# Performance work log

Hardware: AMD Instinct MI355X
Metric: run time of the kernel (lower is better)

## Reference

```python
import jax, jax.numpy as jnp
import numpy as np

B, S, D = 2, 2048, 1024
H, DH = 16, 64
INNER = H * DH  # 1024
FF = 4 * D
WINDOW = 128
EPS = 1e-5
SCALE = DH ** -0.5


def setup_inputs() -> dict:
    key = jax.random.key(0)
    ks = jax.random.split(key, 8)
    s = lambda fan_in: 1.0 / np.sqrt(fan_in)
    return {
        "x": jax.random.normal(ks[0], (B, S, D), dtype=jnp.float32),
        "ln1_g": jnp.ones((D,), jnp.float32),
        "ln1_b": jnp.zeros((D,), jnp.float32),
        "w_qkv": jax.random.uniform(ks[1], (3 * INNER, D), jnp.float32, -s(D), s(D)),
        "w_out": jax.random.uniform(ks[2], (D, INNER), jnp.float32, -s(INNER), s(INNER)),
        "b_out": jnp.zeros((D,), jnp.float32),
        "ln2_g": jnp.ones((D,), jnp.float32),
        "ln2_b": jnp.zeros((D,), jnp.float32),
        "w_ff1": jax.random.uniform(ks[3], (FF, D), jnp.float32, -s(D), s(D)),
        "b_ff1": jnp.zeros((FF,), jnp.float32),
        "w_ff2": jax.random.uniform(ks[4], (D, FF), jnp.float32, -s(FF), s(FF)),
        "b_ff2": jnp.zeros((D,), jnp.float32),
    }


def _layernorm(x, g, b):
    mu = jnp.mean(x, axis=-1, keepdims=True)
    var = jnp.mean(jnp.square(x - mu), axis=-1, keepdims=True)
    return (x - mu) * jax.lax.rsqrt(var + EPS) * g + b


def reference(x, ln1_g, ln1_b, w_qkv, w_out, b_out, ln2_g, ln2_b, w_ff1, b_ff1, w_ff2, b_ff2):
    # --- attention block ---
    residual = x
    h = _layernorm(x, ln1_g, ln1_b)
    qkv = h @ w_qkv.T                             # [B, S, 3*INNER]
    q, k, v = jnp.split(qkv, 3, axis=-1)
    reshape_heads = lambda t: t.reshape(B, S, H, DH).transpose(0, 2, 1, 3)  # [B,H,S,DH]
    q, k, v = map(reshape_heads, (q, k, v))
    q = q * SCALE
    scores = jnp.einsum("bhqd,bhkd->bhqk", q, k)  # dense [B,H,S,S]
    # local sparse pattern: attend iff |i-j| <= window_size
    idx = jnp.arange(S)
    local_mask = jnp.abs(idx[:, None] - idx[None, :]) <= WINDOW  # [S,S] bool
    scores = jnp.where(local_mask[None, None], scores, -jnp.inf)
    attn = jax.nn.softmax(scores, axis=-1)
    attn = jnp.nan_to_num(attn, nan=0.0)
    out = jnp.einsum("bhqk,bhkd->bhqd", attn, v)  # [B,H,S,DH]
    out = out.transpose(0, 2, 1, 3).reshape(B, S, INNER)
    out = out @ w_out.T + b_out                   # dropout inactive (eval)
    x = residual + out
    # --- FFN block ---
    residual = x
    h = _layernorm(x, ln2_g, ln2_b)
    h = jax.nn.gelu(h @ w_ff1.T + b_ff1, approximate=False)
    h = h @ w_ff2.T + b_ff2
    return residual + h
```

## Files before the change

### kernel.cpp

```cpp
#include <hip/hip_runtime.h>
#include <stdint.h>

#define SEQ    2048
#define NB     2
#define DMODEL 1024
#define NHEAD  16
#define HDIM   64
#define FFDIM  4096
#define WIN    128
#define MTOK   (NB*SEQ)

typedef short short8 __attribute__((ext_vector_type(8)));
typedef float f32x4  __attribute__((ext_vector_type(4)));

__device__ __forceinline__ float bf2f(uint16_t h){ return __uint_as_float(((uint32_t)h) << 16); }
__device__ __forceinline__ uint16_t f2bf(float f){
  uint32_t u = __float_as_uint(f);
  u += 0x7fffu + ((u >> 16) & 1u);
  return (uint16_t)(u >> 16);
}

__device__ __forceinline__ float gelu_f(float v){
  float u = 0.7978845608028654f * v * (1.0f + 0.044715f * v * v);
  u = fminf(fmaxf(u, -10.0f), 10.0f);
  const float e = __expf(2.0f * u);
  const float th = (e - 1.0f) / (e + 1.0f);
  return 0.5f * v * (1.0f + th);
}

__device__ __forceinline__ void gl_lds16(const void* g, void* l) {
  __builtin_amdgcn_global_load_lds((const __attribute__((address_space(1))) void*)g,
                                   (__attribute__((address_space(3))) void*)l, 16, 0, 0);
}

__global__ __launch_bounds__(256) void cvtln_kernel(
    const float* __restrict__ s0, const float* __restrict__ s1,
    const float* __restrict__ s2, const float* __restrict__ s3,
    uint16_t* __restrict__ d0, uint16_t* __restrict__ d1,
    uint16_t* __restrict__ d2, uint16_t* __restrict__ d3,
    const float* __restrict__ x, const float* __restrict__ g,
    const float* __restrict__ b, uint16_t* __restrict__ y)
{
  __shared__ float red[8];
  const int t = threadIdx.x;
  if (blockIdx.x < 12288) {
    size_t i = (size_t)blockIdx.x * 256 + t;
    const float* s; uint16_t* d; size_t off;
    if      (i <  768*1024) { s = s0; d = d0; off = i; }
    else if (i < 1024*1024) { s = s1; d = d1; off = i -  768*1024; }
    else if (i < 2048*1024) { s = s2; d = d2; off = i - 1024*1024; }
    else                    { s = s3; d = d3; off = i - 2048*1024; }
    const float4 v = ((const float4*)s)[off];
    uint2 o;
    o.x = (uint32_t)f2bf(v.x) | ((uint32_t)f2bf(v.y) << 16);
    o.y = (uint32_t)f2bf(v.z) | ((uint32_t)f2bf(v.w) << 16);
    ((uint2*)d)[off] = o;
  } else {
    const int row = blockIdx.x - 12288;
    const float4 v = ((const float4*)(x + (size_t)row * DMODEL))[t];
    float s1 = v.x + v.y + v.z + v.w;
    float s2 = v.x*v.x + v.y*v.y + v.z*v.z + v.w*v.w;
    #pragma unroll
    for (int off = 32; off; off >>= 1) { s1 += __shfl_xor(s1, off, 64); s2 += __shfl_xor(s2, off, 64); }
    const int w = t >> 6;
    if ((t & 63) == 0) { red[w] = s1; red[4+w] = s2; }
    __syncthreads();
    s1 = red[0]+red[1]+red[2]+red[3];
    s2 = red[4]+red[5]+red[6]+red[7];
    const float mu = s1 * (1.0f/DMODEL);
    const float var = s2 * (1.0f/DMODEL) - mu*mu;
    const float rs = rsqrtf(var + 1e-5f);
    const float4 gv = ((const float4*)g)[t];
    const float4 bv = ((const float4*)b)[t];
    uint2 o;
    o.x = (uint32_t)f2bf((v.x-mu)*rs*gv.x + bv.x) | ((uint32_t)f2bf((v.y-mu)*rs*gv.y + bv.y) << 16);
    o.y = (uint32_t)f2bf((v.z-mu)*rs*gv.z + bv.z) | ((uint32_t)f2bf((v.w-mu)*rs*gv.w + bv.w) << 16);
    ((uint2*)(y + (size_t)row * DMODEL))[t] = o;
  }
}

__global__ __launch_bounds__(256) void ln_kernel(const float* __restrict__ x,
                                                 const float* __restrict__ g,
                                                 const float* __restrict__ b,
                                                 uint16_t* __restrict__ y)
{
  const int row = blockIdx.x;
  const int t = threadIdx.x;
  const float4 v = ((const float4*)(x + (size_t)row * DMODEL))[t];
  float s1 = v.x + v.y + v.z + v.w;
  float s2 = v.x*v.x + v.y*v.y + v.z*v.z + v.w*v.w;
  #pragma unroll
  for (int off = 32; off; off >>= 1) { s1 += __shfl_xor(s1, off, 64); s2 += __shfl_xor(s2, off, 64); }
  __shared__ float red[8];
  const int w = t >> 6;
  if ((t & 63) == 0) { red[w] = s1; red[4+w] = s2; }
  __syncthreads();
  s1 = red[0]+red[1]+red[2]+red[3];
  s2 = red[4]+red[5]+red[6]+red[7];
  const float mu = s1 * (1.0f/DMODEL);
  const float var = s2 * (1.0f/DMODEL) - mu*mu;
  const float rs = rsqrtf(var + 1e-5f);
  const float4 gv = ((const float4*)g)[t];
  const float4 bv = ((const float4*)b)[t];
  uint2 o;
  o.x = (uint32_t)f2bf((v.x-mu)*rs*gv.x + bv.x) | ((uint32_t)f2bf((v.y-mu)*rs*gv.y + bv.y) << 16);
  o.y = (uint32_t)f2bf((v.z-mu)*rs*gv.z + bv.z) | ((uint32_t)f2bf((v.w-mu)*rs*gv.w + bv.w) << 16);
  ((uint2*)(y + (size_t)row * DMODEL))[t] = o;
}

template<int EPI>
__global__ __launch_bounds__(512, 2) void gemm256(
    const uint16_t* __restrict__ A, const uint16_t* __restrict__ Bm,
    const float* __restrict__ bias, uint16_t* __restrict__ C,
    uint16_t* __restrict__ vt, int M, int N, int K)
{
  __shared__ __align__(16) uint16_t L[4 * 16384];
  const int t = threadIdx.x;
  const int l = t & 63;
  const int w = t >> 6;
  const int wm = w >> 2, wn = w & 3;
  const int GX = gridDim.x;
  const int nblk = GX * gridDim.y;
  const int lin  = blockIdx.y * GX + blockIdx.x;
  const int nid  = (lin & 7) * (nblk >> 3) + (lin >> 3);
  const int row0 = (nid / GX) * 256, col0 = (nid % GX) * 256;
  const int mrow = l & 15, kq = l >> 4;
  const int nt = K >> 5;

  f32x4 acc[8][4];
  #pragma unroll
  for (int i = 0; i < 8; ++i)
    #pragma unroll
    for (int j = 0; j < 4; ++j)
      #pragma unroll
      for (int e = 0; e < 4; ++e) acc[i][j][e] = 0.0f;

  const int sr = t >> 2;
  const int kl = (t & 3) ^ ((t >> 3) & 3);
  const uint16_t* aG = A  + (size_t)(row0 + sr) * K + kl * 8;
  const uint16_t* bG = Bm + (size_t)(col0 + sr) * K + kl * 8;
  char* const lds = (char*)L;
  const int soff = t * 16;

  #define STAGE_A(tt_) { char* d_ = lds + ((tt_) & 3) * 32768 + soff; \
      gl_lds16(aG + (tt_) * 32, d_); \
      gl_lds16(aG + (size_t)128 * K + (tt_) * 32, d_ + 8192); }
  #define STAGE_B(tt_) { char* d_ = lds + ((tt_) & 3) * 32768 + 16384 + soff; \
      gl_lds16(bG + (tt_) * 32, d_); \
      gl_lds16(bG + (size_t)128 * K + (tt_) * 32, d_ + 8192); }

  STAGE_A(0); STAGE_B(0);
  STAGE_A(1); STAGE_B(1);
  STAGE_A(2); STAGE_B(2);
  asm volatile("s_waitcnt vmcnt(8)");
  __builtin_amdgcn_s_barrier();

  const int cphys = (kq ^ ((mrow >> 1) & 3)) << 4;

  for (int tt = 0; tt < nt; ++tt) {
    char* const bufA = lds + (tt & 3) * 32768;
    char* const bufB = bufA + 16384;
    short8 bf[4], af[8];
    #pragma unroll
    for (int ni = 0; ni < 4; ++ni)
      bf[ni] = *(const short8*)(bufB + (wn*64 + ni*16 + mrow) * 64 + cphys);
    #pragma unroll
    for (int mi = 0; mi < 8; ++mi)
      af[mi] = *(const short8*)(bufA + (wm*128 + mi*16 + mrow) * 64 + cphys);
    if (tt + 3 < nt) {
      STAGE_A(tt + 3);
      STAGE_B(tt + 3);
      asm volatile("s_waitcnt vmcnt(8)");
    } else if (tt + 3 == nt) {
      asm volatile("s_waitcnt vmcnt(4)");
    } else if (tt + 2 == nt) {
      asm volatile("s_waitcnt vmcnt(0)");
    }
    __builtin_amdgcn_s_barrier();
    __builtin_amdgcn_s_setprio(1);
    #pragma unroll
    for (int mi = 0; mi < 8; ++mi)
      #pragma unroll
      for (int ni = 0; ni < 4; ++ni)
        acc[mi][ni] = __builtin_amdgcn_mfma_f32_16x16x32_bf16(af[mi], bf[ni], acc[mi][ni], 0, 0, 0);
    __builtin_amdgcn_s_setprio(0);
    __builtin_amdgcn_s_barrier();
  }
  #undef STAGE_A
  #undef STAGE_B

  const int crow = kq * 4;
  if (EPI == 1 && col0 >= 2048) {
    const int hd0 = col0 - 2048 + wn*64 + mrow;
    #pragma unroll
    for (int mi = 0; mi < 8; ++mi) {
      #pragma unroll
      for (int r = 0; r < 4; ++r) {
        const int row = row0 + wm*128 + mi*16 + crow + r;
        const int bb = row >> 11, ss = row & 2047;
        uint16_t* vr = vt + ((size_t)bb << 21) + ss;
        #pragma unroll
        for (int ni = 0; ni < 4; ++ni)
          vr[(size_t)(hd0 + ni*16) << 11] = f2bf(acc[mi][ni][r]);
      }
    }
  } else {
    float bv[4];
    #pragma unroll
    for (int ni = 0; ni < 4; ++ni)
      bv[ni] = (EPI == 2) ? bias[col0 + wn*64 + ni*16 + mrow] : 0.0f;
    #pragma unroll
    for (int mi = 0; mi < 8; ++mi) {
      #pragma unroll
      for (int r = 0; r < 4; ++r) {
        const int row = row0 + wm*128 + mi*16 + crow + r;
        uint16_t* Cr = C + (size_t)row * N + col0 + wn*64 + mrow;
        #pragma unroll
        for (int ni = 0; ni < 4; ++ni) {
          float v = acc[mi][ni][r] + bv[ni];
          if (EPI == 2) v = gelu_f(v);
          Cr[ni*16] = f2bf(v);
        }
      }
    }
  }
}

__global__ __launch_bounds__(512, 2) void gemm128r(
    const uint16_t* __restrict__ A, const uint16_t* __restrict__ Bm,
    const float* __restrict__ bias, const float* __restrict__ res,
    float* __restrict__ out, int M, int N, int K)
{
  __shared__ __align__(16) uint16_t L[4 * 16384];
  const int t = threadIdx.x;
  const int l = t & 63;
  const int w = t >> 6;
  const int wm = w >> 2, wn = w & 3;
  const int GX = gridDim.x;
  const int nblk = GX * gridDim.y;
  const int lin  = blockIdx.y * GX + blockIdx.x;
  const int nid  = (lin & 7) * (nblk >> 3) + (lin >> 3);
  const int row0 = (nid % GX) * 128, col0 = (nid / GX) * 128;
  const int mrow = l & 15, kq = l >> 4;
  const int nt = K >> 6;

  f32x4 acc[4][2];
  #pragma unroll
  for (int i = 0; i < 4; ++i)
    #pragma unroll
    for (int j = 0; j < 2; ++j)
      #pragma unroll
      for (int e = 0; e < 4; ++e) acc[i][j][e] = 0.0f;

  const int sr = t >> 3;
  const int kl = (t & 7) ^ (sr & 7);
  const uint16_t* aG = A  + (size_t)(row0 + sr) * K + kl * 8;
  const uint16_t* bG = Bm + (size_t)(col0 + sr) * K + kl * 8;
  char* const lds = (char*)L;
  const int soff = t * 16;

  #define STAGE_A(tt_) { char* d_ = lds + ((tt_) & 3) * 32768 + soff; \
      gl_lds16(aG + (tt_) * 64, d_); \
      gl_lds16(aG + (size_t)64 * K + (tt_) * 64, d_ + 8192); }
  #define STAGE_B(tt_) { char* d_ = lds + ((tt_) & 3) * 32768 + 16384 + soff; \
      gl_lds16(bG + (tt_) * 64, d_); \
      gl_lds16(bG + (size_t)64 * K + (tt_) * 64, d_ + 8192); }

  STAGE_A(0); STAGE_B(0);
  STAGE_A(1); STAGE_B(1);
  STAGE_A(2); STAGE_B(2);
  asm volatile("s_waitcnt vmcnt(8)");
  __builtin_amdgcn_s_barrier();

  const int pa0 = (kq ^ (mrow & 7)) * 16;
  const int pa1 = ((4 + kq) ^ (mrow & 7)) * 16;

  for (int tt = 0; tt < nt; ++tt) {
    char* const bufA = lds + (tt & 3) * 32768;
    char* const bufB = bufA + 16384;
    short8 af0[4], bf0[2], af1[4], bf1[2];
    #pragma unroll
    for (int ni = 0; ni < 2; ++ni) {
      bf0[ni] = *(const short8*)(bufB + (wn*32 + ni*16 + mrow) * 128 + pa0);
      bf1[ni] = *(const short8*)(bufB + (wn*32 + ni*16 + mrow) * 128 + pa1);
    }
    #pragma unroll
    for (int mi = 0; mi < 4; ++mi) {
      af0[mi] = *(const short8*)(bufA + (wm*64 + mi*16 + mrow) * 128 + pa0);
      af1[mi] = *(const short8*)(bufA + (wm*64 + mi*16 + mrow) * 128 + pa1);
    }
    if (tt + 3 < nt) {
      STAGE_A(tt + 3);
      STAGE_B(tt + 3);
      asm volatile("s_waitcnt vmcnt(8)");
    } else if (tt + 3 == nt) {
      asm volatile("s_waitcnt vmcnt(4)");
    } else if (tt + 2 == nt) {
      asm volatile("s_waitcnt vmcnt(0)");
    }
    __builtin_amdgcn_s_barrier();
    __builtin_amdgcn_s_setprio(1);
    #pragma unroll
    for (int mi = 0; mi < 4; ++mi)
      #pragma unroll
      for (int ni = 0; ni < 2; ++ni)
        acc[mi][ni] = __builtin_amdgcn_mfma_f32_16x16x32_bf16(af0[mi], bf0[ni], acc[mi][ni], 0, 0, 0);
    #pragma unroll
    for (int mi = 0; mi < 4; ++mi)
      #pragma unroll
      for (int ni = 0; ni < 2; ++ni)
        acc[mi][ni] = __builtin_amdgcn_mfma_f32_16x16x32_bf16(af1[mi], bf1[ni], acc[mi][ni], 0, 0, 0);
    __builtin_amdgcn_s_setprio(0);
    __builtin_amdgcn_s_barrier();
  }
  #undef STAGE_A
  #undef STAGE_B

  const int crow = kq * 4;
  float bv[2];
  #pragma unroll
  for (int ni = 0; ni < 2; ++ni)
    bv[ni] = bias[col0 + wn*32 + ni*16 + mrow];
  #pragma unroll
  for (int mi = 0; mi < 4; ++mi)
    #pragma unroll
    for (int r = 0; r < 4; ++r) {
      const int row = row0 + wm*64 + mi*16 + crow + r;
      const size_t base = (size_t)row * N + col0 + wn*32 + mrow;
      #pragma unroll
      for (int ni = 0; ni < 2; ++ni)
        out[base + ni*16] = acc[mi][ni][r] + bv[ni] + res[base + ni*16];
    }
}

#define TQ    32
#define NKT   18
#define NKP   288
#define PSTR  296

__global__ __launch_bounds__(256) void attn_kernel(const uint16_t* __restrict__ qkv,
                                                   const uint16_t* __restrict__ vtg,
                                                   uint16_t* __restrict__ out)
{
  __shared__ __align__(16) uint16_t Qc[8*32*8];
  __shared__ __align__(16) uint16_t Kc[8*288*8];
  __shared__ __align__(16) uint16_t Vc[36*64*8];
  const int t = threadIdx.x, l = t & 63, w = t >> 6;
  const int b = blockIdx.z, hh = blockIdx.y, q0 = blockIdx.x * TQ;
  const int k0 = (q0 - WIN > 0) ? (q0 - WIN) : 0;
  const int kend_ = q0 + TQ + WIN;
  const int kend = (kend_ < SEQ) ? kend_ : SEQ;
  const int nk = kend - k0;

  {
    const size_t vbase = ((size_t)(b*NHEAD + hh) << 17);
    #pragma unroll
    for (int i = 0; i < 9; ++i) {
      const int s = i*256 + t;
      const int c = s >> 6, d = s & 63;
      int off = k0 + c*8; if (off > 2040) off = 2040;
      gl_lds16(vtg + vbase + ((size_t)d << 11) + off, (char*)Vc + (size_t)s*16);
    }
    #pragma unroll
    for (int i = 0; i < 9; ++i) {
      const int s = i*256 + t;
      const int c = s / 288;
      const int j = s - c*288;
      const int js = (j < nk) ? j : (nk - 1);
      gl_lds16(qkv + (size_t)(b*SEQ + k0 + js)*3072 + 1024 + hh*64 + c*8,
               (char*)Kc + (size_t)s*16);
    }
    gl_lds16(qkv + (size_t)(b*SEQ + q0 + (t & 31))*3072 + hh*64 + (t >> 5)*8,
             (char*)Qc + (size_t)t*16);
  }
  __syncthreads();

  const int mrow = l & 15, q4 = l >> 4;
  f32x4 cacc[NKT];
  if (w < 2) {
    const int rb = w * 16;
    const short8 aq0 = *(const short8*)((const char*)Qc + (((q4    )*32 + rb + mrow) << 4));
    const short8 aq1 = *(const short8*)((const char*)Qc + (((4 + q4)*32 + rb + mrow) << 4));
    #pragma unroll
    for (int ct = 0; ct < NKT; ++ct) {
      f32x4 c; c[0]=0.f; c[1]=0.f; c[2]=0.f; c[3]=0.f;
      const short8 b0 = *(const short8*)((const char*)Kc + (((q4    )*288 + ct*16 + mrow) << 4));
      const short8 b1 = *(const short8*)((const char*)Kc + (((4 + q4)*288 + ct*16 + mrow) << 4));
      c = __builtin_amdgcn_mfma_f32_16x16x32_bf16(aq0, b0, c, 0, 0, 0);
      c = __builtin_amdgcn_mfma_f32_16x16x32_bf16(aq1, b1, c, 0, 0, 0);
      cacc[ct] = c;
    }
    #pragma unroll
    for (int r = 0; r < 4; ++r) {
      const int iq = q0 + rb + q4*4 + r;
      float m = -1e30f;
      #pragma unroll
      for (int ct = 0; ct < NKT; ++ct) {
        const int jj = ct*16 + mrow;
        const int j = k0 + jj;
        const bool ok = (jj < nk) && (j >= iq - WIN) && (j <= iq + WIN);
        const float s = ok ? cacc[ct][r] * 0.125f : -1e30f;
        cacc[ct][r] = s;
        m = fmaxf(m, s);
      }
      m = fmaxf(m, __shfl_xor(m, 1, 64));
      m = fmaxf(m, __shfl_xor(m, 2, 64));
      m = fmaxf(m, __shfl_xor(m, 4, 64));
      m = fmaxf(m, __shfl_xor(m, 8, 64));
      float s = 0.f;
      #pragma unroll
      for (int ct = 0; ct < NKT; ++ct) {
        const float e = __expf(cacc[ct][r] - m);
        cacc[ct][r] = e;
        s += e;
      }
      s += __shfl_xor(s, 1, 64);
      s += __shfl_xor(s, 2, 64);
      s += __shfl_xor(s, 4, 64);
      s += __shfl_xor(s, 8, 64);
      const float rinv = 1.0f / s;
      #pragma unroll
      for (int ct = 0; ct < NKT; ++ct)
        cacc[ct][r] *= rinv;
    }
  }
  __syncthreads();

  if (w < 2) {
    uint16_t* Ps = Kc;
    const int rb = w * 16;
    #pragma unroll
    for (int r = 0; r < 4; ++r)
      #pragma unroll
      for (int ct = 0; ct < NKT; ++ct)
        Ps[(rb + q4*4 + r) * PSTR + ct*16 + mrow] = f2bf(cacc[ct][r]);
  }
  __syncthreads();

  {
    const uint16_t* Ps = Kc;
    const int rt = w & 1, dt0 = (w >> 1) * 2;
    f32x4 o0, o1;
    #pragma unroll
    for (int e = 0; e < 4; ++e) { o0[e] = 0.f; o1[e] = 0.f; }
    #pragma unroll
    for (int ks = 0; ks < 9; ++ks) {
      const short8 a  = *(const short8*)((const char*)Ps + (rt*16 + mrow)*(PSTR*2) + ks*64 + q4*16);
      const short8 v0 = *(const short8*)((const char*)Vc + (((ks*4 + q4)*64 + dt0*16 + mrow) << 4));
      const short8 v1 = *(const short8*)((const char*)Vc + (((ks*4 + q4)*64 + (dt0+1)*16 + mrow) << 4));
      o0 = __builtin_amdgcn_mfma_f32_16x16x32_bf16(a, v0, o0, 0, 0, 0);
      o1 = __builtin_amdgcn_mfma_f32_16x16x32_bf16(a, v1, o1, 0, 0, 0);
    }
    #pragma unroll
    for (int r = 0; r < 4; ++r) {
      const int iq = q0 + rt*16 + q4*4 + r;
      const size_t rowoff = (size_t)(b*SEQ + iq) * DMODEL + hh*64;
      out[rowoff + (dt0  )*16 + mrow] = f2bf(o0[r]);
      out[rowoff + (dt0+1)*16 + mrow] = f2bf(o1[r]);
    }
  }
}

extern "C" void kernel_launch(void* const* d_in, const int* in_sizes, int n_in,
                              void* d_out, int out_size, void* d_ws, size_t ws_size,
                              hipStream_t stream)
{
  const float* x    = (const float*)d_in[0];
  const float* ln1g = (const float*)d_in[1];
  const float* ln1b = (const float*)d_in[2];
  const float* wqkv = (const float*)d_in[3];
  const float* wout = (const float*)d_in[4];
  const float* bout = (const float*)d_in[5];
  const float* ln2g = (const float*)d_in[6];
  const float* ln2b = (const float*)d_in[7];
  const float* wff1 = (const float*)d_in[8];
  const float* bff1 = (const float*)d_in[9];
  const float* wff2 = (const float*)d_in[10];
  const float* bff2 = (const float*)d_in[11];
  float* out = (float*)d_out;

  char* ws = (char*)d_ws;
  const size_t MB = (size_t)1 << 20;
  uint16_t* Wqkv = (uint16_t*)(ws);
  uint16_t* Wout = (uint16_t*)(ws +  6*MB);
  uint16_t* Wff1 = (uint16_t*)(ws +  8*MB);
  uint16_t* Wff2 = (uint16_t*)(ws + 16*MB);
  uint16_t* QKV  = (uint16_t*)(ws + 24*MB);
  uint16_t* H1   = (uint16_t*)(ws + 48*MB);
  uint16_t* AT   = H1;
  float*    X2f  = (float*)   (ws + 56*MB);
  uint16_t* H2   = (uint16_t*)(ws + 72*MB);
  uint16_t* FF1  = (uint16_t*)(ws + 24*MB);
  uint16_t* VT   = (uint16_t*)(ws + 80*MB);

  cvtln_kernel<<<16384, 256, 0, stream>>>(wqkv, wout, wff1, wff2,
                                          Wqkv, Wout, Wff1, Wff2,
                                          x, ln1g, ln1b, H1);
  gemm256<1><<<dim3(3072/256, MTOK/256), 512, 0, stream>>>(H1, Wqkv, nullptr, QKV, VT, MTOK, 3072, DMODEL);
  attn_kernel<<<dim3(SEQ/TQ, NHEAD, NB), 256, 0, stream>>>(QKV, VT, AT);
  gemm128r<<<dim3(MTOK/128, DMODEL/128), 512, 0, stream>>>(AT, Wout, bout, x, X2f, MTOK, DMODEL, DMODEL);
  ln_kernel<<<MTOK, 256, 0, stream>>>(X2f, ln2g, ln2b, H2);
  gemm256<2><<<dim3(FFDIM/256, MTOK/256), 512, 0, stream>>>(H2, Wff1, bff1, FF1, nullptr, MTOK, FFDIM, DMODEL);
  gemm128r<<<dim3(MTOK/128, DMODEL/128), 512, 0, stream>>>(FF1, Wff2, bff2, X2f, out, MTOK, DMODEL, FFDIM);
}
```

Before: 313.5 us.

## Split GEMM main loop into two half-phases interleaving A/B staging with MFMA

Restructures the 256x256 bf16 GEMM inner loop into two halves. Each half loads four A fragments, issues one half of the next tile's global->LDS prefetch (A, then B) and runs 16 MFMAs, with barriers placed between the halves. This frees fragment registers and interleaves memory traffic with compute. It also drops the XCD-aware block-index remapping in favour of a plain blockIdx mapping, which may hurt L2 locality, and it doubles the number of barriers per K-step.

After: 318.4 us. About the same (+1.6%).

```diff
diff --git a/kernel.cpp b/kernel.cpp
--- a/kernel.cpp
+++ b/kernel.cpp
@@ -31,6 +31,12 @@
 __device__ __forceinline__ void gl_lds16(const void* g, void* l) {
   __builtin_amdgcn_global_load_lds((const __attribute__((address_space(1))) void*)g,
                                    (__attribute__((address_space(3))) void*)l, 16, 0, 0);
+}
+
+__device__ __forceinline__ void BARM() {
+  asm volatile("" ::: "memory");
+  __builtin_amdgcn_s_barrier();
+  asm volatile("" ::: "memory");
 }
 
 __global__ __launch_bounds__(256) void cvtln_kernel(
@@ -119,11 +125,7 @@
   const int l = t & 63;
   const int w = t >> 6;
   const int wm = w >> 2, wn = w & 3;
-  const int GX = gridDim.x;
-  const int nblk = GX * gridDim.y;
-  const int lin  = blockIdx.y * GX + blockIdx.x;
-  const int nid  = (lin & 7) * (nblk >> 3) + (lin >> 3);
-  const int row0 = (nid / GX) * 256, col0 = (nid % GX) * 256;
+  const int row0 = blockIdx.y * 256, col0 = blockIdx.x * 256;
   const int mrow = l & 15, kq = l >> 4;
   const int nt = K >> 5;
 
@@ -152,39 +154,51 @@
   STAGE_A(0); STAGE_B(0);
   STAGE_A(1); STAGE_B(1);
   STAGE_A(2); STAGE_B(2);
-  asm volatile("s_waitcnt vmcnt(8)");
-  __builtin_amdgcn_s_barrier();
+  asm volatile("s_waitcnt vmcnt(8)" ::: "memory");
+  BARM();
 
   const int cphys = (kq ^ ((mrow >> 1) & 3)) << 4;
 
   for (int tt = 0; tt < nt; ++tt) {
     char* const bufA = lds + (tt & 3) * 32768;
     char* const bufB = bufA + 16384;
-    short8 bf[4], af[8];
+    short8 bf[4], af[4];
     #pragma unroll
     for (int ni = 0; ni < 4; ++ni)
       bf[ni] = *(const short8*)(bufB + (wn*64 + ni*16 + mrow) * 64 + cphys);
     #pragma unroll
-    for (int mi = 0; mi < 8; ++mi)
+    for (int mi = 0; mi < 4; ++mi)
       af[mi] = *(const short8*)(bufA + (wm*128 + mi*16 + mrow) * 64 + cphys);
-    if (tt + 3 < nt) {
-      STAGE_A(tt + 3);
-      STAGE_B(tt + 3);
-      asm volatile("s_waitcnt vmcnt(8)");
-    } else if (tt + 3 == nt) {
-      asm volatile("s_waitcnt vmcnt(4)");
-    } else if (tt + 2 == nt) {
-      asm volatile("s_waitcnt vmcnt(0)");
-    }
-    __builtin_amdgcn_s_barrier();
+    if (tt + 3 < nt) STAGE_A(tt + 3);
+    BARM();
     __builtin_amdgcn_s_setprio(1);
     #pragma unroll
-    for (int mi = 0; mi < 8; ++mi)
+    for (int mi = 0; mi < 4; ++mi)
       #pragma unroll
       for (int ni = 0; ni < 4; ++ni)
         acc[mi][ni] = __builtin_amdgcn_mfma_f32_16x16x32_bf16(af[mi], bf[ni], acc[mi][ni], 0, 0, 0);
     __builtin_amdgcn_s_setprio(0);
-    __builtin_amdgcn_s_barrier();
+    BARM();
+    #pragma unroll
+    for (int mi = 0; mi < 4; ++mi)
+      af[mi] = *(const short8*)(bufA + (wm*128 + (mi+4)*16 + mrow) * 64 + cphys);
+    if (tt + 3 < nt) {
+      STAGE_B(tt + 3);
+      asm volatile("s_waitcnt vmcnt(8)" ::: "memory");
+    } else if (tt + 3 == nt) {
+      asm volatile("s_waitcnt vmcnt(4)" ::: "memory");
+    } else if (tt + 2 == nt) {
+      asm volatile("s_waitcnt vmcnt(0)" ::: "memory");
+    }
+    BARM();
+    __builtin_amdgcn_s_setprio(1);
+    #pragma unroll
+    for (int mi = 0; mi < 4; ++mi)
+      #pragma unroll
+      for (int ni = 0; ni < 4; ++ni)
+        acc[mi+4][ni] = __builtin_amdgcn_mfma_f32_16x16x32_bf16(af[mi], bf[ni], acc[mi+4][ni], 0, 0, 0);
+    __builtin_amdgcn_s_setprio(0);
+    BARM();
   }
   #undef STAGE_A
   #undef STAGE_B
```
